# Kernel tuning notes

Measured on AMD Instinct MI355X. Metric: run time of the kernel, lower is better.

The kernel has to match this reference:

```python
import jax, jax.numpy as jnp
import numpy as np


def _conv1x1(x, w, b=None):
    # x: (B, Cin, H, W), w: (Cout, Cin)
    y = jnp.einsum('oi,bihw->bohw', w, x)
    if b is not None:
        y = y + b[None, :, None, None]
    return y


def _adaptive_avg_pool(x, ps):
    # faithful torch AdaptiveAvgPool2d: bin i covers [floor(i*H/ps), ceil((i+1)*H/ps))
    H, W = x.shape[-2], x.shape[-1]
    rows = []
    for i in range(ps):
        hs, he = (i * H) // ps, -((-(i + 1) * H) // ps)
        cols = []
        for j in range(ps):
            ws, we = (j * W) // ps, -((-(j + 1) * W) // ps)
            cols.append(x[..., hs:he, ws:we].mean((-2, -1)))
        rows.append(jnp.stack(cols, -1))
    return jnp.stack(rows, -2)


def _bilinear(x, oh, ow, align_corners):
    H, W = x.shape[-2], x.shape[-1]
    def coords(o, I):
        if align_corners:
            c = jnp.arange(o, dtype=jnp.float32) * (float(I - 1) / max(o - 1, 1))
        else:
            c = jnp.clip((jnp.arange(o, dtype=jnp.float32) + 0.5) * (float(I) / o) - 0.5, 0.0, float(I - 1))
        i0 = jnp.floor(c).astype(jnp.int32)
        i1 = jnp.minimum(i0 + 1, I - 1)
        return i0, i1, (c - i0).astype(x.dtype)
    y0, y1, wy = coords(oh, H)
    x0, x1, wx = coords(ow, W)
    top = x[..., y0, :]
    bot = x[..., y1, :]
    a, b = top[..., x0], top[..., x1]
    c, d = bot[..., x0], bot[..., x1]
    r0 = a * (1 - wx) + b * wx
    r1 = c * (1 - wx) + d * wx
    return r0 * (1 - wy[:, None]) + r1 * wy[:, None]


def setup_inputs() -> dict:
    key = jax.random.key(0)
    ks = jax.random.split(key, 32)
    Cin, C, B, H, W = 512, 64, 2, 48, 48
    def rnd(k, shape, s=0.05):
        return jax.random.normal(k, shape, jnp.float32) * s
    inp = {
        'x': jax.random.normal(ks[0], (B, Cin, H, W), jnp.float32),
        'w_gc0': rnd(ks[1], (C, Cin)), 'b_gc0': rnd(ks[2], (C,)),
        'w_gc1': rnd(ks[3], (C, Cin)), 'b_gc1': rnd(ks[4], (C,)),
        'w_gc2': rnd(ks[5], (C, Cin)), 'b_gc2': rnd(ks[6], (C,)),
        'w_gc3': rnd(ks[7], (C, Cin)), 'b_gc3': rnd(ks[8], (C,)),
        'w_q': rnd(ks[9], (C // 8, C)), 'b_q': rnd(ks[10], (C // 8,)),
        'w_k': rnd(ks[11], (C // 8, C)), 'b_k': rnd(ks[12], (C // 8,)),
        'w_v': rnd(ks[13], (C, C)), 'b_v': rnd(ks[14], (C,)),
        'gamma': jnp.ones((1,), jnp.float32),
        'w_se1': rnd(ks[15], (C, C)), 'w_se2': rnd(ks[16], (C, C)),
        'w_se3': rnd(ks[17], (C, C)), 'w_se4': rnd(ks[18], (C, C)),
        'w_out0': rnd(ks[19], (256, 4 * C)), 'b_out0': rnd(ks[20], (256,)),
        'w_out1': rnd(ks[21], (128, 4 * C)), 'b_out1': rnd(ks[22], (128,)),
        'w_out2': rnd(ks[23], (64, 4 * C)), 'b_out2': rnd(ks[24], (64,)),
        'w_out3': rnd(ks[25], (64, 4 * C)), 'b_out3': rnd(ks[26], (64,)),
    }
    return inp


def reference(x, w_gc0, b_gc0, w_gc1, b_gc1, w_gc2, b_gc2, w_gc3, b_gc3,
              w_q, b_q, w_k, b_k, w_v, b_v, gamma,
              w_se1, w_se2, w_se3, w_se4,
              w_out0, b_out0, w_out1, b_out1, w_out2, b_out2, w_out3, b_out3):
    B, _, H, W = x.shape
    # multi-scale pooled branches (pool sizes 1,3,5), bilinear up w/ align_corners=True
    gcs = []
    for ps, w_, b_ in ((1, w_gc0, b_gc0), (3, w_gc1, b_gc1), (5, w_gc2, b_gc2)):
        p = jax.nn.relu(_conv1x1(_adaptive_avg_pool(x, ps), w_, b_))
        gcs.append(_bilinear(p, H, W, True))
    # full-resolution SA branch
    s = jax.nn.relu(_conv1x1(x, w_gc3, b_gc3))
    N = H * W
    q = _conv1x1(s, w_q, b_q).reshape(B, -1, N)   # (B, C/8, N)
    k = _conv1x1(s, w_k, b_k).reshape(B, -1, N)
    v = _conv1x1(s, w_v, b_v).reshape(B, -1, N)   # (B, C, N)
    attn = jax.nn.softmax(jnp.einsum('bcm,bcn->bmn', q, k), axis=-1)  # (B, N, N)
    sa = jnp.einsum('bcn,bmn->bcm', v, attn).reshape(s.shape)
    sa = gamma * sa + s
    # SE channel-attention weights (note original's cross pairing of branches)
    gap = lambda t: t.mean((2, 3), keepdims=True)
    y3 = _conv1x1(gap(gcs[0]), w_se4)
    y2 = _conv1x1(gap(gcs[1]), w_se3)
    y1 = _conv1x1(gap(gcs[2]), w_se2)
    y0 = _conv1x1(gap(sa), w_se1)
    wgt = jnp.concatenate([y0, y1, y2, y3], axis=2)      # (B, 64, 4, 1)
    wgt = jax.nn.softmax(jax.nn.sigmoid(wgt), axis=2)
    fused = jnp.concatenate([
        wgt[:, :, 0:1, :] * gcs[0],
        wgt[:, :, 1:2, :] * gcs[1],
        wgt[:, :, 2:3, :] * gcs[2],
        wgt[:, :, 3:4, :] * sa,
    ], axis=1)                                            # (B, 256, H, W)
    outs = []
    for sc, w_, b_ in ((2, w_out0, b_out0), (4, w_out1, b_out1), (8, w_out2, b_out2), (16, w_out3, b_out3)):
        y = jax.nn.relu(_conv1x1(fused, w_, b_))
        outs.append(_bilinear(y, H * sc, W * sc, False))  # nn.Upsample default align_corners=False
    return tuple(outs)
```

## Files before the change

kernel.cpp:

```cpp
#include <hip/hip_runtime.h>
#include <hip/hip_bf16.h>
#include <hip/hip_fp16.h>


typedef __attribute__((ext_vector_type(8))) short short8;
typedef __attribute__((ext_vector_type(4))) float f32x4;

#define GLOAD_LDS(gsrc, ldst) \
  __builtin_amdgcn_global_load_lds((const __attribute__((address_space(1))) void*)(gsrc), \
                                   (__attribute__((address_space(3))) void*)(ldst), 16, 0, 0)

static constexpr size_t OFF_P1 = 0;
static constexpr size_t OFF_P3 = OFF_P1 + 2*512;
static constexpr size_t OFF_P5 = OFF_P3 + 18*512;
static constexpr size_t OFF_G0 = OFF_P5 + 50*512;
static constexpr size_t OFF_G1 = OFF_G0 + 2*64;
static constexpr size_t OFF_G2 = OFF_G1 + 18*64;
static constexpr size_t OFF_S  = OFF_G2 + 50*64;
static constexpr size_t OFF_Q  = OFF_S  + 294912;
static constexpr size_t OFF_K  = OFF_Q  + 36864;
static constexpr size_t OFF_V  = OFF_K  + 36864;
static constexpr size_t OFF_SA = OFF_V  + 294912;
static constexpr size_t OFF_GC = OFF_SA + 294912;
static constexpr size_t OFF_MEAN = OFF_GC + 3*294912;
static constexpr size_t OFF_WGT  = OFF_MEAN + 512;
static constexpr size_t OFF_Y0 = OFF_WGT + 512;
static constexpr size_t OFF_Y1 = OFF_Y0 + 1179648;
static constexpr size_t OFF_Y2 = OFF_Y1 + 589824;
static constexpr size_t OFF_Y3 = OFF_Y2 + 294912;

__global__ __launch_bounds__(256) void k_pool(const float* __restrict__ x, float* __restrict__ wsp){
  __shared__ float pl[2304];
  __shared__ float red[4];
  int bc = blockIdx.x;
  int b = bc >> 9, cin = bc & 511;
  const float* src = x + (size_t)bc * 2304;
  int t = threadIdx.x;
  float ls = 0.f;
  #pragma unroll
  for (int j = 0; j < 9; j++){ int i = t + j*256; float v = src[i]; pl[i] = v; ls += v; }
  #pragma unroll
  for (int o = 32; o; o >>= 1) ls += __shfl_xor(ls, o);
  if ((t & 63) == 0) red[t >> 6] = ls;
  __syncthreads();
  if (t == 0) wsp[OFF_P1 + (size_t)b*512 + cin] = (red[0]+red[1]+red[2]+red[3]) * (1.f/2304.f);
  if (t < 9){
    int ry = t/3, rx = t%3; float sm = 0.f;
    for (int yy = 0; yy < 16; yy++)
      for (int xx = 0; xx < 16; xx++) sm += pl[(ry*16+yy)*48 + rx*16+xx];
    wsp[OFF_P3 + ((size_t)b*9 + t)*512 + cin] = sm * (1.f/256.f);
  } else if (t < 34){
    int j = t - 9; int ry = j/5, rx = j%5;
    int hs = (ry*48)/5, he = ((ry+1)*48+4)/5, cs = (rx*48)/5, ce = ((rx+1)*48+4)/5;
    float sm = 0.f;
    for (int yy = hs; yy < he; yy++)
      for (int xx = cs; xx < ce; xx++) sm += pl[yy*48+xx];
    wsp[OFF_P5 + ((size_t)b*25 + j)*512 + cin] = sm / (float)((he-hs)*(ce-cs));
  }
}

__global__ __launch_bounds__(256) void k_gcconv(
    const float* __restrict__ w0, const float* __restrict__ b0,
    const float* __restrict__ w1, const float* __restrict__ b1,
    const float* __restrict__ w2, const float* __restrict__ b2,
    float* __restrict__ wsp){
  int col = blockIdx.x;
  const float* w; const float* bias; const float* pool; float* dst;
  if (col < 2){ w = w0; bias = b0; pool = wsp + OFF_P1 + (size_t)col*512; dst = wsp + OFF_G0 + (size_t)col*64; }
  else if (col < 20){ int c = col-2;  w = w1; bias = b1; pool = wsp + OFF_P3 + (size_t)c*512; dst = wsp + OFF_G1 + (size_t)c*64; }
  else              { int c = col-20; w = w2; bias = b2; pool = wsp + OFF_P5 + (size_t)c*512; dst = wsp + OFF_G2 + (size_t)c*64; }
  int t = threadIdx.x; int r = t >> 2, qd = t & 3;
  const float* wr = w + (size_t)r*512 + qd*128;
  const float* pr = pool + qd*128;
  float acc = 0.f;
  #pragma unroll 8
  for (int k = 0; k < 128; k += 4){
    float4 wv = *(const float4*)(wr + k); float4 pv = *(const float4*)(pr + k);
    acc += wv.x*pv.x + wv.y*pv.y + wv.z*pv.z + wv.w*pv.w;
  }
  acc += __shfl_xor(acc, 1); acc += __shfl_xor(acc, 2);
  if (qd == 0) dst[r] = fmaxf(acc + bias[r], 0.f);
}

__global__ __launch_bounds__(256) void k_sgemm_qkv(const float* __restrict__ x,
    const float* __restrict__ w, const float* __restrict__ bias,
    const float* __restrict__ wq, const float* __restrict__ bq,
    const float* __restrict__ wk, const float* __restrict__ bk,
    const float* __restrict__ wv, const float* __restrict__ bv,
    float* __restrict__ wsp){
  __shared__ __align__(16) float wt[64][66];
  __shared__ __align__(16) float xs[64][32];
  __shared__ __align__(16) float s_lds[64][36];
  __shared__ float wq_lds[80][64];
  __shared__ float bqkv[80];
  int cb = blockIdx.x;
  int b = cb / 72, hw0 = (cb - b*72)*32;
  int tid = threadIdx.x;
  int wv_ = tid >> 6, lane = tid & 63;
  for (int i = tid; i < 5120; i += 256){
    int row = i >> 6, k = i & 63;
    wq_lds[row][k] = (row < 8) ? wq[(size_t)row*64 + k]
                   : (row < 16) ? wk[(size_t)(row-8)*64 + k]
                                : wv[(size_t)(row-16)*64 + k];
  }
  if (tid < 80) bqkv[tid] = (tid < 8) ? bq[tid] : (tid < 16) ? bk[tid-8] : bv[tid-16];
  int sr = tid >> 2, sseg = tid & 3;
  int cc0 = (tid & 7)*4, r0 = (tid >> 3)*2;
  const float* xb = x + (size_t)b*512*2304 + hw0;
  float acc[2][4] = {};
  for (int kc = 0; kc < 512; kc += 64){
    __syncthreads();
    {
      int rr0 = wv_*16 + (lane >> 3);
      const float* g0 = xb + (size_t)(kc + rr0)*2304 + (lane & 7)*4;
      const float* g1 = xb + (size_t)(kc + rr0 + 8)*2304 + (lane & 7)*4;
      GLOAD_LDS(g0, &xs[wv_*16][0]);
      GLOAD_LDS(g1, &xs[wv_*16 + 8][0]);
    }
    #pragma unroll
    for (int i = 0; i < 16; i += 4){
      float4 v = *(const float4*)(w + (size_t)sr*512 + kc + sseg*16 + i);
      wt[sseg*16+i+0][sr]=v.x; wt[sseg*16+i+1][sr]=v.y;
      wt[sseg*16+i+2][sr]=v.z; wt[sseg*16+i+3][sr]=v.w;
    }
    __syncthreads();
    #pragma unroll 4
    for (int k = 0; k < 64; k++){
      float2 wv2 = *(const float2*)&wt[k][r0];
      float4 xv = *(const float4*)&xs[k][cc0];
      acc[0][0]+=wv2.x*xv.x; acc[0][1]+=wv2.x*xv.y; acc[0][2]+=wv2.x*xv.z; acc[0][3]+=wv2.x*xv.w;
      acc[1][0]+=wv2.y*xv.x; acc[1][1]+=wv2.y*xv.y; acc[1][2]+=wv2.y*xv.z; acc[1][3]+=wv2.y*xv.w;
    }
  }
  #pragma unroll
  for (int i = 0; i < 2; i++){
    float bi = bias[r0+i];
    float4 o;
    o.x = fmaxf(acc[i][0]+bi, 0.f); o.y = fmaxf(acc[i][1]+bi, 0.f);
    o.z = fmaxf(acc[i][2]+bi, 0.f); o.w = fmaxf(acc[i][3]+bi, 0.f);
    *(float4*)(wsp + OFF_S + ((size_t)b*64 + r0+i)*2304 + hw0 + cc0) = o;
    *(float4*)&s_lds[r0+i][cc0] = o;
  }
  __syncthreads();
  int col = tid & 31, rgrp = tid >> 5;
  float a2[10];
  #pragma unroll
  for (int i = 0; i < 10; i++) a2[i] = bqkv[rgrp*10 + i];
  for (int k = 0; k < 64; k++){
    float sv = s_lds[k][col];
    #pragma unroll
    for (int i = 0; i < 10; i++) a2[i] += wq_lds[rgrp*10 + i][k]*sv;
  }
  __hip_bfloat16* Vb = reinterpret_cast<__hip_bfloat16*>(wsp + OFF_V);
  int hw = hw0 + col;
  #pragma unroll
  for (int i = 0; i < 10; i++){
    int r = rgrp*10 + i;
    if (r < 8)       wsp[OFF_Q + (size_t)b*18432 + (size_t)r*2304 + hw] = a2[i];
    else if (r < 16) wsp[OFF_K + (size_t)b*18432 + (size_t)(r-8)*2304 + hw] = a2[i];
    else             Vb[(size_t)b*147456 + (size_t)(r-16)*2304 + hw] = __float2bfloat16(a2[i]);
  }
}

__global__ __launch_bounds__(256) void k_attn(float* __restrict__ wsp, const float* __restrict__ gamma){
  int mb = blockIdx.x * 16;
  int b  = blockIdx.y;
  int t = threadIdx.x;
  int w = t >> 6, lane = t & 63;
  int arow = lane & 15, kg = lane >> 4;
  __shared__ float qs[16][8];
  __shared__ __align__(16) unsigned short plds[16][2312];
  __shared__ float redM[4][16], redS[4][16];
  __shared__ float tile[16][68];
  const float* Qp = wsp + OFF_Q + (size_t)b*18432;
  const float* Kp = wsp + OFF_K + (size_t)b*18432;
  if (t < 128) qs[t>>3][t&7] = Qp[(size_t)(t&7)*2304 + mb + (t>>3)];
  __syncthreads();
  float k8[9][8];
  #pragma unroll
  for (int j = 0; j < 9; j++){
    int n = j*256 + t;
    #pragma unroll
    for (int c = 0; c < 8; c++) k8[j][c] = Kp[(size_t)c*2304 + n];
  }
  float mx[16], ssum[16];
  #pragma unroll
  for (int m = 0; m < 16; m++){
    float q0=qs[m][0], q1=qs[m][1], q2=qs[m][2], q3=qs[m][3];
    float q4=qs[m][4], q5=qs[m][5], q6=qs[m][6], q7=qs[m][7];
    float lmx = -1e30f, ls = 0.f;
    #pragma unroll
    for (int j = 0; j < 9; j++){
      float l = q0*k8[j][0]+q1*k8[j][1]+q2*k8[j][2]+q3*k8[j][3]
              + q4*k8[j][4]+q5*k8[j][5]+q6*k8[j][6]+q7*k8[j][7];
      __half hv = __float2half(l);
      plds[m][j*256 + t] = __half_as_ushort(hv);
      float mo = lmx;
      lmx = fmaxf(lmx, l);
      ls = ls*__expf(mo - lmx) + __expf(l - lmx);
    }
    mx[m] = lmx; ssum[m] = ls;
  }
  #pragma unroll
  for (int m = 0; m < 16; m++){
    float M = mx[m], S = ssum[m];
    #pragma unroll
    for (int off = 32; off; off >>= 1){
      float oM = __shfl_xor(M, off), oS = __shfl_xor(S, off);
      float nM = fmaxf(M, oM);
      S = S*__expf(M - nM) + oS*__expf(oM - nM);
      M = nM;
    }
    if (lane == 0){ redM[w][m] = M; redS[w][m] = S; }
  }
  __syncthreads();
  float Mf[16], invS[16];
  #pragma unroll
  for (int m = 0; m < 16; m++){
    float M0 = redM[0][m], M1 = redM[1][m], M2 = redM[2][m], M3 = redM[3][m];
    float M = fmaxf(fmaxf(M0, M1), fmaxf(M2, M3));
    float S = redS[0][m]*__expf(M0-M) + redS[1][m]*__expf(M1-M)
            + redS[2][m]*__expf(M2-M) + redS[3][m]*__expf(M3-M);
    Mf[m] = M; invS[m] = 1.f/S;
  }
  const short* Vb = (const short*)(wsp + OFF_V) + (size_t)b*147456 + (size_t)(w*16 + arow)*2304;
  f32x4 acc = {0.f, 0.f, 0.f, 0.f};
  for (int j = 0; j < 9; j++){
    int n = j*256 + t;
    #pragma unroll
    for (int m = 0; m < 16; m++){
      float l = __half2float(__ushort_as_half(plds[m][n]));
      float p = __expf(l - Mf[m]) * invS[m];
      __hip_bfloat16 pb = __float2bfloat16(p);
      plds[m][n] = *(unsigned short*)&pb;
    }
    __syncthreads();
    #pragma unroll
    for (int ks = 0; ks < 8; ks++){
      int nb = j*256 + ks*32 + kg*8;
      short8 a  = *(const short8*)&plds[arow][nb];
      short8 bv = *(const short8*)(Vb + nb);
      acc = __builtin_amdgcn_mfma_f32_16x16x32_bf16(a, bv, acc, 0, 0, 0);
    }
  }
  #pragma unroll
  for (int r = 0; r < 4; r++) tile[kg*4 + r][w*16 + arow] = acc[r];
  __syncthreads();
  int c = t >> 2, mq = t & 3;
  float g = gamma[0];
  const float* Sp = wsp + OFF_S + (size_t)b*147456 + (size_t)c*2304 + mb + mq*4;
  float4 s4 = *(const float4*)Sp;
  float4 o;
  o.x = g*tile[mq*4+0][c] + s4.x;
  o.y = g*tile[mq*4+1][c] + s4.y;
  o.z = g*tile[mq*4+2][c] + s4.z;
  o.w = g*tile[mq*4+3][c] + s4.w;
  *(float4*)(wsp + OFF_SA + (size_t)b*147456 + (size_t)c*2304 + mb + mq*4) = o;
}

__global__ __launch_bounds__(256) void k_gcup(float* __restrict__ wsp){
  int px = blockIdx.x*256 + threadIdx.x;
  int pb = blockIdx.y;
  int c = pb & 63, b = (pb >> 6) & 1, t = pb >> 7;
  int oy = px / 48, ox = px - oy*48;
  int ps; const float* g;
  if (t == 0){ ps = 1; g = wsp + OFF_G0 + (size_t)b*64; }
  else if (t == 1){ ps = 3; g = wsp + OFF_G1 + (size_t)b*9*64; }
  else { ps = 5; g = wsp + OFF_G2 + (size_t)b*25*64; }
  float scale = (ps - 1) / 47.f;
  float cy = oy*scale, cx = ox*scale;
  int y0 = (int)cy, x0 = (int)cx;
  float wy = cy - y0, wx = cx - x0;
  int y1 = min(y0+1, ps-1), x1 = min(x0+1, ps-1);
  float a  = g[(y0*ps+x0)*64 + c], bq = g[(y0*ps+x1)*64 + c];
  float cc = g[(y1*ps+x0)*64 + c], d  = g[(y1*ps+x1)*64 + c];
  float v = (a*(1.f-wx) + bq*wx)*(1.f-wy) + (cc*(1.f-wx) + d*wx)*wy;
  wsp[OFF_GC + (((size_t)t*2 + b)*64 + c)*2304 + px] = v;
}

__global__ __launch_bounds__(256) void k_gap(float* __restrict__ wsp){
  __shared__ float red[4];
  int blk = blockIdx.x; int c = blk & 63, b = blk >> 6;
  const float* src = wsp + OFF_SA + ((size_t)b*64 + c)*2304;
  float s = 0.f;
  for (int i = threadIdx.x; i < 2304; i += 256) s += src[i];
  #pragma unroll
  for (int o = 32; o; o >>= 1) s += __shfl_xor(s, o);
  if ((threadIdx.x & 63) == 0) red[threadIdx.x >> 6] = s;
  __syncthreads();
  if (threadIdx.x == 0)
    wsp[OFF_MEAN + (size_t)b*64 + c] = (red[0]+red[1]+red[2]+red[3]) * (1.f/2304.f);
}

__global__ __launch_bounds__(256) void k_se(
    const float* __restrict__ w_se1, const float* __restrict__ w_se2,
    const float* __restrict__ w_se3, const float* __restrict__ w_se4,
    float* __restrict__ wsp){
  int b = blockIdx.x; int tid = threadIdx.x;
  int g = tid >> 6, c = tid & 63;
  __shared__ float mean_lds[4][64];
  float mv;
  if (g == 0){
    mv = wsp[OFF_MEAN + (size_t)b*64 + c];
  } else if (g == 3){
    mv = wsp[OFF_G0 + (size_t)b*64 + c];
  } else if (g == 2){
    float w3[3] = {0.f,0.f,0.f};
    for (int o = 0; o < 48; o++){
      float cc = o*(2.f/47.f); int i0 = (int)cc; float f = cc - i0;
      int i1 = min(i0+1, 2);
      w3[i0] += 1.f - f; w3[i1] += f;
    }
    float s = 0.f;
    for (int sy = 0; sy < 3; sy++)
      for (int sx = 0; sx < 3; sx++)
        s += w3[sy]*w3[sx]*wsp[OFF_G1 + ((size_t)b*9 + sy*3 + sx)*64 + c];
    mv = s * (1.f/(48.f*48.f));
  } else {
    float w5[5] = {0.f,0.f,0.f,0.f,0.f};
    for (int o = 0; o < 48; o++){
      float cc = o*(4.f/47.f); int i0 = (int)cc; float f = cc - i0;
      int i1 = min(i0+1, 4);
      w5[i0] += 1.f - f; w5[i1] += f;
    }
    float s = 0.f;
    for (int sy = 0; sy < 5; sy++)
      for (int sx = 0; sx < 5; sx++)
        s += w5[sy]*w5[sx]*wsp[OFF_G2 + ((size_t)b*25 + sy*5 + sx)*64 + c];
    mv = s * (1.f/(48.f*48.f));
  }
  mean_lds[g][c] = mv;
  __syncthreads();
  const float* w = (g == 0) ? w_se1 : (g == 1) ? w_se2 : (g == 2) ? w_se3 : w_se4;
  float acc = 0.f;
  for (int j = 0; j < 64; j++) acc += w[(size_t)c*64 + j]*mean_lds[g][j];
  float sg = 1.f / (1.f + __expf(-acc));
  __shared__ float sh[4][64];
  sh[g][c] = sg;
  __syncthreads();
  float a0 = sh[0][c], a1 = sh[1][c], a2 = sh[2][c], a3 = sh[3][c];
  float mxv = fmaxf(fmaxf(a0, a1), fmaxf(a2, a3));
  float e = __expf(sg - mxv);
  float sum = __expf(a0-mxv) + __expf(a1-mxv) + __expf(a2-mxv) + __expf(a3-mxv);
  wsp[OFF_WGT + ((size_t)b*4 + g)*64 + c] = e / sum;
}

__global__ __launch_bounds__(256) void k_outgemm(
    const float* __restrict__ w0, const float* __restrict__ b0,
    const float* __restrict__ w1, const float* __restrict__ b1,
    const float* __restrict__ w2, const float* __restrict__ b2,
    const float* __restrict__ w3, const float* __restrict__ b3,
    float* __restrict__ wsp){
  __shared__ __align__(16) float wt[64][68];
  __shared__ __align__(16) float xsh[64][64];
  __shared__ float wg[256];
  int cb = blockIdx.x, rb = blockIdx.y;
  int b = cb / 36, hw0 = (cb - b*36)*64;
  const float* wsrc; const float* bsrc; size_t dstoff; int dstC; int row0;
  if (rb < 4){ wsrc = w0 + (size_t)rb*64*256; bsrc = b0 + rb*64; dstoff = OFF_Y0; dstC = 256; row0 = rb*64; }
  else if (rb < 6){ wsrc = w1 + (size_t)(rb-4)*64*256; bsrc = b1 + (rb-4)*64; dstoff = OFF_Y1; dstC = 128; row0 = (rb-4)*64; }
  else if (rb == 6){ wsrc = w2; bsrc = b2; dstoff = OFF_Y2; dstC = 64; row0 = 0; }
  else { wsrc = w3; bsrc = b3; dstoff = OFF_Y3; dstC = 64; row0 = 0; }
  int tid = threadIdx.x;
  int wv_ = tid >> 6, lane = tid & 63;
  wg[tid] = wsp[OFF_WGT + (size_t)b*256 + tid];
  int sr = tid >> 2, sseg = tid & 3;
  int cc0 = (tid & 15)*4, r0 = (tid >> 4)*4;
  float acc[4][4] = {};
  for (int kc = 0; kc < 256; kc += 64){
    __syncthreads();
    {
      int gidx = kc >> 6;
      size_t srcbase = (gidx < 3) ? OFF_GC + ((size_t)(gidx*2 + b))*147456
                                  : OFF_SA + (size_t)b*147456;
      const float* gb = wsp + srcbase + hw0 + (lane & 15)*4;
      int rr = wv_*16 + (lane >> 4);
      #pragma unroll
      for (int i = 0; i < 4; i++)
        GLOAD_LDS(gb + (size_t)(rr + i*4)*2304, &xsh[wv_*16 + i*4][0]);
    }
    #pragma unroll
    for (int i = 0; i < 16; i += 4){
      float4 v = *(const float4*)(wsrc + (size_t)sr*256 + kc + sseg*16 + i);
      int kl = sseg*16 + i;
      wt[kl+0][sr]=v.x*wg[kc+kl+0]; wt[kl+1][sr]=v.y*wg[kc+kl+1];
      wt[kl+2][sr]=v.z*wg[kc+kl+2]; wt[kl+3][sr]=v.w*wg[kc+kl+3];
    }
    __syncthreads();
    #pragma unroll 4
    for (int k = 0; k < 64; k++){
      float4 wv = *(const float4*)&wt[k][r0];
      float4 xv = *(const float4*)&xsh[k][cc0];
      acc[0][0]+=wv.x*xv.x; acc[0][1]+=wv.x*xv.y; acc[0][2]+=wv.x*xv.z; acc[0][3]+=wv.x*xv.w;
      acc[1][0]+=wv.y*xv.x; acc[1][1]+=wv.y*xv.y; acc[1][2]+=wv.y*xv.z; acc[1][3]+=wv.y*xv.w;
      acc[2][0]+=wv.z*xv.x; acc[2][1]+=wv.z*xv.y; acc[2][2]+=wv.z*xv.z; acc[2][3]+=wv.z*xv.w;
      acc[3][0]+=wv.w*xv.x; acc[3][1]+=wv.w*xv.y; acc[3][2]+=wv.w*xv.z; acc[3][3]+=wv.w*xv.w;
    }
  }
  #pragma unroll
  for (int i = 0; i < 4; i++){
    float bi = bsrc[r0+i];
    float4 o;
    o.x = fmaxf(acc[i][0]+bi, 0.f); o.y = fmaxf(acc[i][1]+bi, 0.f);
    o.z = fmaxf(acc[i][2]+bi, 0.f); o.w = fmaxf(acc[i][3]+bi, 0.f);
    *(float4*)(wsp + dstoff + ((size_t)b*dstC + row0 + r0 + i)*2304 + hw0 + cc0) = o;
  }
}

template<int SC>
__device__ __forceinline__ void up_one(int idx, const float* __restrict__ src, float* __restrict__ dst){
  constexpr int OW = 48*SC, OH = 48*SC;
  constexpr int WQ = OW/4;
  int q = idx % WQ; int rest = idx / WQ;
  int oy = rest % OH; int pc = rest / OH;
  const float* sp = src + (size_t)pc * 2304;
  float cy = fminf(fmaxf((oy + 0.5f)*(1.0f/SC) - 0.5f, 0.f), 47.f);
  int y0 = (int)cy;
  float wy = cy - y0;
  int y1 = min(y0+1, 47);
  const float* r0 = sp + y0*48; const float* r1 = sp + y1*48;
  float outv[4];
  #pragma unroll
  for (int i = 0; i < 4; i++){
    int ox = q*4 + i;
    float cx = fminf(fmaxf((ox + 0.5f)*(1.0f/SC) - 0.5f, 0.f), 47.f);
    int x0 = (int)cx; float wx = cx - x0; int x1 = min(x0+1, 47);
    float a  = r0[x0]*(1.f-wx) + r0[x1]*wx;
    float bq = r1[x0]*(1.f-wx) + r1[x1]*wx;
    outv[i] = a*(1.f-wy) + bq*wy;
  }
  f32x4 o; o[0] = outv[0]; o[1] = outv[1]; o[2] = outv[2]; o[3] = outv[3];
  f32x4* dp = (f32x4*)(dst + (size_t)pc*OH*OW + (size_t)oy*OW + q*4);
  __builtin_nontemporal_store(o, dp);
}

__global__ __launch_bounds__(256) void k_upsample_all(const float* __restrict__ wsp, float* __restrict__ out){
  int t = blockIdx.x*256 + threadIdx.x;
  if (t < 1179648)       up_one<2>(t,           wsp + OFF_Y0, out);
  else if (t < 3538944)  up_one<4>(t - 1179648, wsp + OFF_Y1, out + 4718592);
  else if (t < 8257536)  up_one<8>(t - 3538944, wsp + OFF_Y2, out + 14155776);
  else                   up_one<16>(t - 8257536, wsp + OFF_Y3, out + 33030144);
}

extern "C" void kernel_launch(void* const* d_in, const int* in_sizes, int n_in,
                              void* d_out, int out_size, void* d_ws, size_t ws_size,
                              hipStream_t stream){
  const float* x     = (const float*)d_in[0];
  const float* w_gc0 = (const float*)d_in[1];
  const float* b_gc0 = (const float*)d_in[2];
  const float* w_gc1 = (const float*)d_in[3];
  const float* b_gc1 = (const float*)d_in[4];
  const float* w_gc2 = (const float*)d_in[5];
  const float* b_gc2 = (const float*)d_in[6];
  const float* w_gc3 = (const float*)d_in[7];
  const float* b_gc3 = (const float*)d_in[8];
  const float* w_q   = (const float*)d_in[9];
  const float* b_q   = (const float*)d_in[10];
  const float* w_k   = (const float*)d_in[11];
  const float* b_k   = (const float*)d_in[12];
  const float* w_v   = (const float*)d_in[13];
  const float* b_v   = (const float*)d_in[14];
  const float* gamma = (const float*)d_in[15];
  const float* w_se1 = (const float*)d_in[16];
  const float* w_se2 = (const float*)d_in[17];
  const float* w_se3 = (const float*)d_in[18];
  const float* w_se4 = (const float*)d_in[19];
  const float* w_out0 = (const float*)d_in[20];
  const float* b_out0 = (const float*)d_in[21];
  const float* w_out1 = (const float*)d_in[22];
  const float* b_out1 = (const float*)d_in[23];
  const float* w_out2 = (const float*)d_in[24];
  const float* b_out2 = (const float*)d_in[25];
  const float* w_out3 = (const float*)d_in[26];
  const float* b_out3 = (const float*)d_in[27];
  float* wsp = (float*)d_ws;
  float* out = (float*)d_out;

  k_pool     <<<1024, 256, 0, stream>>>(x, wsp);
  k_gcconv   <<<70,   256, 0, stream>>>(w_gc0,b_gc0,w_gc1,b_gc1,w_gc2,b_gc2, wsp);
  k_sgemm_qkv<<<144,  256, 0, stream>>>(x, w_gc3, b_gc3, w_q,b_q,w_k,b_k,w_v,b_v, wsp);
  k_attn     <<<dim3(144,2), 256, 0, stream>>>(wsp, gamma);
  k_gcup     <<<dim3(9,384), 256, 0, stream>>>(wsp);
  k_gap      <<<128,  256, 0, stream>>>(wsp);
  k_se       <<<2,    256, 0, stream>>>(w_se1,w_se2,w_se3,w_se4, wsp);
  k_outgemm  <<<dim3(72,8), 256, 0, stream>>>(w_out0,b_out0,w_out1,b_out1,w_out2,b_out2,w_out3,b_out3, wsp);
  k_upsample_all<<<105984, 256, 0, stream>>>(wsp, out);
}
```

Measured before the change: 217.1 us.

## Merge small kernels into shared launches to cut launch count

Folds the pooled-feature 1x1 conv blocks into the attention launch as extra blocks, and moves the global-average-pool reduction into the SE kernel. The SE blocks are then appended to the global-context upsample launch. This takes the pipeline from nine launches to six, removing launch overhead and inter-kernel gaps for several tiny kernels. The trade-off is that the SE blocks now reduce all 64 channels per batch with a single block, which may leave a serial tail at the end of that launch.

```diff
diff --git a/kernel.cpp b/kernel.cpp
--- a/kernel.cpp
+++ b/kernel.cpp
@@ -57,29 +57,6 @@
       for (int xx = cs; xx < ce; xx++) sm += pl[yy*48+xx];
     wsp[OFF_P5 + ((size_t)b*25 + j)*512 + cin] = sm / (float)((he-hs)*(ce-cs));
   }
-}
-
-__global__ __launch_bounds__(256) void k_gcconv(
-    const float* __restrict__ w0, const float* __restrict__ b0,
-    const float* __restrict__ w1, const float* __restrict__ b1,
-    const float* __restrict__ w2, const float* __restrict__ b2,
-    float* __restrict__ wsp){
-  int col = blockIdx.x;
-  const float* w; const float* bias; const float* pool; float* dst;
-  if (col < 2){ w = w0; bias = b0; pool = wsp + OFF_P1 + (size_t)col*512; dst = wsp + OFF_G0 + (size_t)col*64; }
-  else if (col < 20){ int c = col-2;  w = w1; bias = b1; pool = wsp + OFF_P3 + (size_t)c*512; dst = wsp + OFF_G1 + (size_t)c*64; }
-  else              { int c = col-20; w = w2; bias = b2; pool = wsp + OFF_P5 + (size_t)c*512; dst = wsp + OFF_G2 + (size_t)c*64; }
-  int t = threadIdx.x; int r = t >> 2, qd = t & 3;
-  const float* wr = w + (size_t)r*512 + qd*128;
-  const float* pr = pool + qd*128;
-  float acc = 0.f;
-  #pragma unroll 8
-  for (int k = 0; k < 128; k += 4){
-    float4 wv = *(const float4*)(wr + k); float4 pv = *(const float4*)(pr + k);
-    acc += wv.x*pv.x + wv.y*pv.y + wv.z*pv.z + wv.w*pv.w;
-  }
-  acc += __shfl_xor(acc, 1); acc += __shfl_xor(acc, 2);
-  if (qd == 0) dst[r] = fmaxf(acc + bias[r], 0.f);
 }
 
 __global__ __launch_bounds__(256) void k_sgemm_qkv(const float* __restrict__ x,
@@ -162,19 +139,23 @@
   }
 }
 
-__global__ __launch_bounds__(256) void k_attn(float* __restrict__ wsp, const float* __restrict__ gamma){
-  int mb = blockIdx.x * 16;
-  int b  = blockIdx.y;
+struct AttnSmem {
+  float qs[16][8];
+  unsigned short plds[16][2312];
+  float redM[4][16], redS[4][16];
+  float tile[16][68];
+};
+
+__device__ void attn_body(char* smem_raw, int blk, float* __restrict__ wsp, const float* __restrict__ gamma){
+  AttnSmem& s = *reinterpret_cast<AttnSmem*>(smem_raw);
+  int mb = (blk % 144) * 16;
+  int b  = blk / 144;
   int t = threadIdx.x;
   int w = t >> 6, lane = t & 63;
   int arow = lane & 15, kg = lane >> 4;
-  __shared__ float qs[16][8];
-  __shared__ __align__(16) unsigned short plds[16][2312];
-  __shared__ float redM[4][16], redS[4][16];
-  __shared__ float tile[16][68];
   const float* Qp = wsp + OFF_Q + (size_t)b*18432;
   const float* Kp = wsp + OFF_K + (size_t)b*18432;
-  if (t < 128) qs[t>>3][t&7] = Qp[(size_t)(t&7)*2304 + mb + (t>>3)];
+  if (t < 128) s.qs[t>>3][t&7] = Qp[(size_t)(t&7)*2304 + mb + (t>>3)];
   __syncthreads();
   float k8[9][8];
   #pragma unroll
@@ -186,15 +167,15 @@
   float mx[16], ssum[16];
   #pragma unroll
   for (int m = 0; m < 16; m++){
-    float q0=qs[m][0], q1=qs[m][1], q2=qs[m][2], q3=qs[m][3];
-    float q4=qs[m][4], q5=qs[m][5], q6=qs[m][6], q7=qs[m][7];
+    float q0=s.qs[m][0], q1=s.qs[m][1], q2=s.qs[m][2], q3=s.qs[m][3];
+    float q4=s.qs[m][4], q5=s.qs[m][5], q6=s.qs[m][6], q7=s.qs[m][7];
     float lmx = -1e30f, ls = 0.f;
     #pragma unroll
     for (int j = 0; j < 9; j++){
       float l = q0*k8[j][0]+q1*k8[j][1]+q2*k8[j][2]+q3*k8[j][3]
               + q4*k8[j][4]+q5*k8[j][5]+q6*k8[j][6]+q7*k8[j][7];
       __half hv = __float2half(l);
-      plds[m][j*256 + t] = __half_as_ushort(hv);
+      s.plds[m][j*256 + t] = __half_as_ushort(hv);
       float mo = lmx;
       lmx = fmaxf(lmx, l);
       ls = ls*__expf(mo - lmx) + __expf(l - lmx);
@@ -211,16 +192,16 @@
       S = S*__expf(M - nM) + oS*__expf(oM - nM);
       M = nM;
     }
-    if (lane == 0){ redM[w][m] = M; redS[w][m] = S; }
+    if (lane == 0){ s.redM[w][m] = M; s.redS[w][m] = S; }
   }
   __syncthreads();
   float Mf[16], invS[16];
   #pragma unroll
   for (int m = 0; m < 16; m++){
-    float M0 = redM[0][m], M1 = redM[1][m], M2 = redM[2][m], M3 = redM[3][m];
+    float M0 = s.redM[0][m], M1 = s.redM[1][m], M2 = s.redM[2][m], M3 = s.redM[3][m];
     float M = fmaxf(fmaxf(M0, M1), fmaxf(M2, M3));
-    float S = redS[0][m]*__expf(M0-M) + redS[1][m]*__expf(M1-M)
-            + redS[2][m]*__expf(M2-M) + redS[3][m]*__expf(M3-M);
+    float S = s.redS[0][m]*__expf(M0-M) + s.redS[1][m]*__expf(M1-M)
+            + s.redS[2][m]*__expf(M2-M) + s.redS[3][m]*__expf(M3-M);
     Mf[m] = M; invS[m] = 1.f/S;
   }
   const short* Vb = (const short*)(wsp + OFF_V) + (size_t)b*147456 + (size_t)(w*16 + arow)*2304;
@@ -229,38 +210,70 @@
     int n = j*256 + t;
     #pragma unroll
     for (int m = 0; m < 16; m++){
-      float l = __half2float(__ushort_as_half(plds[m][n]));
+      float l = __half2float(__ushort_as_half(s.plds[m][n]));
       float p = __expf(l - Mf[m]) * invS[m];
       __hip_bfloat16 pb = __float2bfloat16(p);
-      plds[m][n] = *(unsigned short*)&pb;
+      s.plds[m][n] = *(unsigned short*)&pb;
     }
     __syncthreads();
     #pragma unroll
     for (int ks = 0; ks < 8; ks++){
       int nb = j*256 + ks*32 + kg*8;
-      short8 a  = *(const short8*)&plds[arow][nb];
+      short8 a  = *(const short8*)&s.plds[arow][nb];
       short8 bv = *(const short8*)(Vb + nb);
       acc = __builtin_amdgcn_mfma_f32_16x16x32_bf16(a, bv, acc, 0, 0, 0);
     }
   }
   #pragma unroll
-  for (int r = 0; r < 4; r++) tile[kg*4 + r][w*16 + arow] = acc[r];
+  for (int r = 0; r < 4; r++) s.tile[kg*4 + r][w*16 + arow] = acc[r];
   __syncthreads();
   int c = t >> 2, mq = t & 3;
   float g = gamma[0];
   const float* Sp = wsp + OFF_S + (size_t)b*147456 + (size_t)c*2304 + mb + mq*4;
   float4 s4 = *(const float4*)Sp;
   float4 o;
-  o.x = g*tile[mq*4+0][c] + s4.x;
-  o.y = g*tile[mq*4+1][c] + s4.y;
-  o.z = g*tile[mq*4+2][c] + s4.z;
-  o.w = g*tile[mq*4+3][c] + s4.w;
+  o.x = g*s.tile[mq*4+0][c] + s4.x;
+  o.y = g*s.tile[mq*4+1][c] + s4.y;
+  o.z = g*s.tile[mq*4+2][c] + s4.z;
+  o.w = g*s.tile[mq*4+3][c] + s4.w;
   *(float4*)(wsp + OFF_SA + (size_t)b*147456 + (size_t)c*2304 + mb + mq*4) = o;
 }
 
-__global__ __launch_bounds__(256) void k_gcup(float* __restrict__ wsp){
-  int px = blockIdx.x*256 + threadIdx.x;
-  int pb = blockIdx.y;
+__device__ void gcconv_body(int col,
+    const float* __restrict__ w0, const float* __restrict__ b0,
+    const float* __restrict__ w1, const float* __restrict__ b1,
+    const float* __restrict__ w2, const float* __restrict__ b2,
+    float* __restrict__ wsp){
+  const float* w; const float* bias; const float* pool; float* dst;
+  if (col < 2){ w = w0; bias = b0; pool = wsp + OFF_P1 + (size_t)col*512; dst = wsp + OFF_G0 + (size_t)col*64; }
+  else if (col < 20){ int c = col-2;  w = w1; bias = b1; pool = wsp + OFF_P3 + (size_t)c*512; dst = wsp + OFF_G1 + (size_t)c*64; }
+  else              { int c = col-20; w = w2; bias = b2; pool = wsp + OFF_P5 + (size_t)c*512; dst = wsp + OFF_G2 + (size_t)c*64; }
+  int t = threadIdx.x; int r = t >> 2, qd = t & 3;
+  const float* wr = w + (size_t)r*512 + qd*128;
+  const float* pr = pool + qd*128;
+  float acc = 0.f;
+  #pragma unroll 8
+  for (int k = 0; k < 128; k += 4){
+    float4 wv = *(const float4*)(wr + k); float4 pv = *(const float4*)(pr + k);
+    acc += wv.x*pv.x + wv.y*pv.y + wv.z*pv.z + wv.w*pv.w;
+  }
+  acc += __shfl_xor(acc, 1); acc += __shfl_xor(acc, 2);
+  if (qd == 0) dst[r] = fmaxf(acc + bias[r], 0.f);
+}
+
+__global__ __launch_bounds__(256) void k_attn_gcconv(float* __restrict__ wsp, const float* __restrict__ gamma,
+    const float* __restrict__ w0, const float* __restrict__ b0,
+    const float* __restrict__ w1, const float* __restrict__ b1,
+    const float* __restrict__ w2, const float* __restrict__ b2){
+  __shared__ __align__(16) char smem[sizeof(AttnSmem)];
+  int bx = blockIdx.x;
+  if (bx < 288) attn_body(smem, bx, wsp, gamma);
+  else          gcconv_body(bx - 288, w0, b0, w1, b1, w2, b2, wsp);
+}
+
+__device__ void gcup_body(int u, float* __restrict__ wsp){
+  int px = (u % 9)*256 + threadIdx.x;
+  int pb = u / 9;
   int c = pb & 63, b = (pb >> 6) & 1, t = pb >> 7;
   int oy = px / 48, ox = px - oy*48;
   int ps; const float* g;
@@ -278,30 +291,28 @@
   wsp[OFF_GC + (((size_t)t*2 + b)*64 + c)*2304 + px] = v;
 }
 
-__global__ __launch_bounds__(256) void k_gap(float* __restrict__ wsp){
-  __shared__ float red[4];
-  int blk = blockIdx.x; int c = blk & 63, b = blk >> 6;
-  const float* src = wsp + OFF_SA + ((size_t)b*64 + c)*2304;
-  float s = 0.f;
-  for (int i = threadIdx.x; i < 2304; i += 256) s += src[i];
-  #pragma unroll
-  for (int o = 32; o; o >>= 1) s += __shfl_xor(s, o);
-  if ((threadIdx.x & 63) == 0) red[threadIdx.x >> 6] = s;
-  __syncthreads();
-  if (threadIdx.x == 0)
-    wsp[OFF_MEAN + (size_t)b*64 + c] = (red[0]+red[1]+red[2]+red[3]) * (1.f/2304.f);
-}
-
-__global__ __launch_bounds__(256) void k_se(
+__device__ void se_body(int b,
     const float* __restrict__ w_se1, const float* __restrict__ w_se2,
     const float* __restrict__ w_se3, const float* __restrict__ w_se4,
     float* __restrict__ wsp){
-  int b = blockIdx.x; int tid = threadIdx.x;
+  __shared__ float msa[64];
+  __shared__ float mean_lds[4][64];
+  __shared__ float sh[4][64];
+  int tid = threadIdx.x;
+  int wv_ = tid >> 6, lane = tid & 63;
+  for (int r = wv_; r < 64; r += 4){
+    const float* src = wsp + OFF_SA + (size_t)b*147456 + (size_t)r*2304;
+    float s = 0.f;
+    for (int i = lane; i < 2304; i += 64) s += src[i];
+    #pragma unroll
+    for (int o = 32; o; o >>= 1) s += __shfl_xor(s, o);
+    if (lane == 0) msa[r] = s * (1.f/2304.f);
+  }
+  __syncthreads();
   int g = tid >> 6, c = tid & 63;
-  __shared__ float mean_lds[4][64];
   float mv;
   if (g == 0){
-    mv = wsp[OFF_MEAN + (size_t)b*64 + c];
+    mv = msa[c];
   } else if (g == 3){
     mv = wsp[OFF_G0 + (size_t)b*64 + c];
   } else if (g == 2){
@@ -335,7 +346,6 @@
   float acc = 0.f;
   for (int j = 0; j < 64; j++) acc += w[(size_t)c*64 + j]*mean_lds[g][j];
   float sg = 1.f / (1.f + __expf(-acc));
-  __shared__ float sh[4][64];
   sh[g][c] = sg;
   __syncthreads();
   float a0 = sh[0][c], a1 = sh[1][c], a2 = sh[2][c], a3 = sh[3][c];
@@ -343,6 +353,14 @@
   float e = __expf(sg - mxv);
   float sum = __expf(a0-mxv) + __expf(a1-mxv) + __expf(a2-mxv) + __expf(a3-mxv);
   wsp[OFF_WGT + ((size_t)b*4 + g)*64 + c] = e / sum;
+}
+
+__global__ __launch_bounds__(256) void k_gcup_se(float* __restrict__ wsp,
+    const float* __restrict__ w_se1, const float* __restrict__ w_se2,
+    const float* __restrict__ w_se3, const float* __restrict__ w_se4){
+  int bx = blockIdx.x;
+  if (bx < 3456) gcup_body(bx, wsp);
+  else           se_body(bx - 3456, w_se1, w_se2, w_se3, w_se4, wsp);
 }
 
 __global__ __launch_bounds__(256) void k_outgemm(
@@ -476,13 +494,10 @@
   float* wsp = (float*)d_ws;
   float* out = (float*)d_out;
 
-  k_pool     <<<1024, 256, 0, stream>>>(x, wsp);
-  k_gcconv   <<<70,   256, 0, stream>>>(w_gc0,b_gc0,w_gc1,b_gc1,w_gc2,b_gc2, wsp);
-  k_sgemm_qkv<<<144,  256, 0, stream>>>(x, w_gc3, b_gc3, w_q,b_q,w_k,b_k,w_v,b_v, wsp);
-  k_attn     <<<dim3(144,2), 256, 0, stream>>>(wsp, gamma);
-  k_gcup     <<<dim3(9,384), 256, 0, stream>>>(wsp);
-  k_gap      <<<128,  256, 0, stream>>>(wsp);
-  k_se       <<<2,    256, 0, stream>>>(w_se1,w_se2,w_se3,w_se4, wsp);
-  k_outgemm  <<<dim3(72,8), 256, 0, stream>>>(w_out0,b_out0,w_out1,b_out1,w_out2,b_out2,w_out3,b_out3, wsp);
+  k_pool      <<<1024, 256, 0, stream>>>(x, wsp);
+  k_sgemm_qkv <<<144,  256, 0, stream>>>(x, w_gc3, b_gc3, w_q,b_q,w_k,b_k,w_v,b_v, wsp);
+  k_attn_gcconv<<<358, 256, 0, stream>>>(wsp, gamma, w_gc0,b_gc0,w_gc1,b_gc1,w_gc2,b_gc2);
+  k_gcup_se   <<<3458, 256, 0, stream>>>(wsp, w_se1,w_se2,w_se3,w_se4);
+  k_outgemm   <<<dim3(72,8), 256, 0, stream>>>(w_out0,b_out0,w_out1,b_out1,w_out2,b_out2,w_out3,b_out3, wsp);
   k_upsample_all<<<105984, 256, 0, stream>>>(wsp, out);
 }
```

After: 371.6 us. 1.71x slower.
